# Kernel optimization log

Hardware: AMD Instinct MI355X
Metric: run time of the kernel (lower is better)

Reference implementation:

```python
import jax, jax.numpy as jnp
import numpy as np

WS = 11          # window_size
SIGMA = 1.5
PAD = (WS - 1) // 2
C1 = (0.01 * 1.0) ** 2
C2 = (0.03 * 1.0) ** 2


def _gaussian_kernel2d():
    # kornia-style: 1D gaussian over window, normalized, outer product
    x = jnp.arange(WS, dtype=jnp.float32) - WS // 2
    g = jnp.exp(-(x ** 2) / (2.0 * SIGMA ** 2))
    g = g / jnp.sum(g)
    return jnp.outer(g, g)  # [WS, WS]


def _filter2d(x, k2d):
    # depthwise 2D filter with reflect ('same') padding, as kornia.filter2D
    b, c, h, w = x.shape
    xp = jnp.pad(x, ((0, 0), (0, 0), (PAD, PAD), (PAD, PAD)), mode='reflect')
    kern = jnp.broadcast_to(k2d.astype(x.dtype), (c, 1, WS, WS))
    return jax.lax.conv_general_dilated(
        xp, kern, window_strides=(1, 1), padding='VALID',
        feature_group_count=c,
        dimension_numbers=('NCHW', 'OIHW', 'NCHW'))


def setup_inputs() -> dict:
    key = jax.random.key(0)
    k1, k2 = jax.random.split(key)
    inp = jax.random.normal(k1, (16, 1, 1024, 1024), dtype=jnp.float32)
    tgt = jax.random.uniform(k2, (16, 1, 1024, 1024), dtype=jnp.float32)
    return {"input": inp, "target": tgt}


def reference(input, target):
    k2d = _gaussian_kernel2d()
    img1 = jax.nn.sigmoid(input)  # logsigmoid(x).exp() == sigmoid(x)
    img2 = target

    mu1 = _filter2d(img1, k2d)
    mu2 = _filter2d(img2, k2d)
    mu1_sq = mu1 * mu1
    mu2_sq = mu2 * mu2
    mu1_mu2 = mu1 * mu2

    sigma1_sq = _filter2d(img1 * img1, k2d) - mu1_sq
    sigma2_sq = _filter2d(img2 * img2, k2d) - mu2_sq
    sigma12 = _filter2d(img1 * img2, k2d) - mu1_mu2

    ssim_map = ((2.0 * mu1_mu2 + C1) * (2.0 * sigma12 + C2)) / (
        (mu1_sq + mu2_sq + C1) * (sigma1_sq + sigma2_sq + C2))
    loss = jnp.clip(1.0 - ssim_map, 0.0, 1.0) / 2.0
    return jnp.mean(loss)  # reduction='mean'
```

## Files before the change

### kernel.cpp

```cpp
#include <hip/hip_runtime.h>
#include <math.h>


typedef __attribute__((ext_vector_type(2))) float f2;

#define H_IMG 1024
#define W_IMG 1024
#define N_IMG 16
#define TILE_W 256
#define TILE_H 128
#define PADR 5
#define LDS_S2 268

constexpr float GW[11] = {
    0.00102838f, 0.00759877f, 0.03600077f, 0.10936069f, 0.21300553f,
    0.26601172f,
    0.21300553f, 0.10936069f, 0.03600077f, 0.00759877f, 0.00102838f};

__device__ __forceinline__ int reflect_i(int i, int n) {
    i = (i < 0) ? -i : i;
    i = (i >= n) ? (2 * n - 2 - i) : i;
    return i;
}

__device__ __forceinline__ float fast_sigmoid(float x) {
    return __builtin_amdgcn_rcpf(1.0f + __expf(-x));
}

__device__ __forceinline__ void ssim_emit(
    f2 mu, f2 sq, float e12, float& loss_sum)
{
    const float mu1 = mu.x, mu2 = mu.y;
    const float mu1s = mu1 * mu1;
    const float mu2s = mu2 * mu2;
    const float mu12 = mu1 * mu2;
    const float s1  = sq.x - mu1s;
    const float s2  = sq.y - mu2s;
    const float s12 = e12  - mu12;
    const float C1 = 1e-4f, C2 = 9e-4f;
    const float num = (2.0f * mu12 + C1) * (2.0f * s12 + C2);
    const float den = (mu1s + mu2s + C1) * (s1 + s2 + C2);
    float l = 1.0f - num * __builtin_amdgcn_rcpf(den);
    l = fminf(fmaxf(l, 0.0f), 1.0f) * 0.5f;
    loss_sum += l;
}

template<int NR>
__device__ __forceinline__ void load_group(
    const float* __restrict__ A, const float* __restrict__ B,
    int y_start, int gb, int c0, int c1, int tid,
    float (&pa)[11], float (&pb)[11], float (&pa2)[11], float (&pb2)[11])
{
#pragma unroll
    for (int r = 0; r < NR; ++r) {
        const int yy = reflect_i(y_start + gb + r, H_IMG);
        const size_t ro = (size_t)yy * W_IMG;
        pa[r] = A[ro + c0];
        pb[r] = B[ro + c0];
        if (tid < 2 * PADR) {
            pa2[r] = A[ro + c1];
            pb2[r] = B[ro + c1];
        }
    }
}

template<int NR>
__device__ __forceinline__ void write_group(
    f2 (*__restrict__ buf)[LDS_S2], int tid,
    const float (&pa)[11], const float (&pb)[11],
    const float (&pa2)[11], const float (&pb2)[11])
{
#pragma unroll
    for (int r = 0; r < NR; ++r) {
        buf[r][tid] = (f2){fast_sigmoid(pa[r]), pb[r]};
        if (tid < 2 * PADR)
            buf[r][TILE_W + tid] = (f2){fast_sigmoid(pa2[r]), pb2[r]};
    }
}

template<int NR, bool GUARD>
__device__ __forceinline__ void process_group(
    const f2 (*__restrict__ buf)[LDS_S2], int tid,
    f2 (&vAB)[11], f2 (&vSQ)[11], float (&vX)[11], float& loss_sum)
{
#pragma unroll
    for (int r = 0; r < NR; ++r) {
        f2 hAB = (f2)(0.0f), hSQ = (f2)(0.0f);
        float hab = 0.0f;
#pragma unroll
        for (int k = 0; k < 11; ++k) {
            const f2 v   = buf[r][tid + k];
            const f2 wa2 = ((f2)(GW[k])) * v;
            hAB += wa2;
            hSQ  = __builtin_elementwise_fma(wa2, v, hSQ);
            hab  = fmaf(wa2.x, v.y, hab);
        }
#pragma unroll
        for (int j = 0; j < 11; ++j) {
            if (!(GUARD && j > r)) {
                const int s = (r - j + 22) % 11;
                const f2 w2 = (f2)(GW[j]);
                vAB[s] = __builtin_elementwise_fma(w2, hAB, vAB[s]);
                vSQ[s] = __builtin_elementwise_fma(w2, hSQ, vSQ[s]);
                vX[s]  = fmaf(GW[j], hab, vX[s]);
            }
        }
        if (!GUARD || r == 10) {
            const int s = (r + 1) % 11;
            ssim_emit(vAB[s], vSQ[s], vX[s], loss_sum);
            vAB[s] = (f2)(0.0f); vSQ[s] = (f2)(0.0f); vX[s] = 0.0f;
        }
    }
}

__global__ __launch_bounds__(256, 2) void ssim_main(
    const float* __restrict__ inp, const float* __restrict__ tgt,
    float* __restrict__ out)
{
    __shared__ f2 bufs[2][11][LDS_S2];
    __shared__ float red[4];

    const int tid = threadIdx.x;
    const int blk = blockIdx.x;
    const int b   = blk >> 5;
    const int rem = blk & 31;
    const int cx  = rem & 3;
    const int ry  = rem >> 2;
    const int x0  = cx * TILE_W;
    const int y0  = ry * TILE_H;

    const float* __restrict__ A = inp + (size_t)b * (H_IMG * (size_t)W_IMG);
    const float* __restrict__ B = tgt + (size_t)b * (H_IMG * (size_t)W_IMG);

    const int c0 = reflect_i(x0 - PADR + tid, W_IMG);
    const int c1 = (tid < 2 * PADR) ? reflect_i(x0 + TILE_W - PADR + tid, W_IMG) : 0;

    f2 vAB[11], vSQ[11];
    float vX[11];
#pragma unroll
    for (int j = 0; j < 11; ++j) {
        vAB[j] = (f2)(0.0f); vSQ[j] = (f2)(0.0f); vX[j] = 0.0f;
    }
    float pa[11], pb[11], pa2[11], pb2[11];
    float loss_sum = 0.0f;

    const int y_start = y0 - PADR;

    load_group<11>(A, B, y_start, 0, c0, c1, tid, pa, pb, pa2, pb2);
    write_group<11>(bufs[0], tid, pa, pb, pa2, pb2);
    load_group<11>(A, B, y_start, 11, c0, c1, tid, pa, pb, pa2, pb2);
    __syncthreads();
    process_group<11, true>(bufs[0], tid, vAB, vSQ, vX, loss_sum);

#pragma unroll 1
    for (int g = 1; g <= 11; ++g) {
        f2 (*cur)[LDS_S2] = bufs[g & 1];
        write_group<11>(cur, tid, pa, pb, pa2, pb2);
        if (g <= 10)
            load_group<11>(A, B, y_start, (g + 1) * 11, c0, c1, tid, pa, pb, pa2, pb2);
        else
            load_group<6>(A, B, y_start, 132, c0, c1, tid, pa, pb, pa2, pb2);
        __syncthreads();
        process_group<11, false>(cur, tid, vAB, vSQ, vX, loss_sum);
    }

    write_group<6>(bufs[0], tid, pa, pb, pa2, pb2);
    __syncthreads();
    process_group<6, false>(bufs[0], tid, vAB, vSQ, vX, loss_sum);

#pragma unroll
    for (int off = 32; off > 0; off >>= 1)
        loss_sum += __shfl_down(loss_sum, off, 64);
    const int wave = tid >> 6;
    if ((tid & 63) == 0) red[wave] = loss_sum;
    __syncthreads();
    if (tid == 0) {
        const float s = red[0] + red[1] + red[2] + red[3];
        atomicAdd(out, s * (1.0f / ((float)N_IMG * H_IMG * W_IMG)));
    }
}

extern "C" void kernel_launch(void* const* d_in, const int* in_sizes, int n_in,
                              void* d_out, int out_size, void* d_ws, size_t ws_size,
                              hipStream_t stream) {
    const float* inp = (const float*)d_in[0];
    const float* tgt = (const float*)d_in[1];
    float* out = (float*)d_out;

    hipMemsetAsync(out, 0, sizeof(float), stream);

    const int grid = N_IMG * 4 * (H_IMG / TILE_H);
    ssim_main<<<grid, 256, 0, stream>>>(inp, tgt, out);
}
```

Before: 182.7 us.

## Stream rows via global_load_lds DMA into a 12-slot ring with smaller tiles

Replaces register-staged global loads with direct global-to-LDS DMA into double-buffered 6-row slabs. Each slab is then repacked, with the sigmoid applied, into a 12-slot ring buffer that feeds the separable Gaussian accumulation. Tile height drops from 128 to 32 rows, quadrupling the block count, and the occupancy hint rises to 3 blocks per CU. This is meant to free registers, overlap memory with compute and improve latency hiding. In exchange, each block recomputes a larger 10-row halo relative to its height, and the manual waitcnt/barrier sequencing adds correctness risk.

Result: slower. 258.7 us (+41.6%).

```diff
diff --git a/kernel.cpp b/kernel.cpp
--- a/kernel.cpp
+++ b/kernel.cpp
@@ -8,9 +8,11 @@
 #define W_IMG 1024
 #define N_IMG 16
 #define TILE_W 256
-#define TILE_H 128
+#define TILE_H 32
 #define PADR 5
-#define LDS_S2 268
+#define RING_S 268
+#define SLAB_S 268
+#define NSLOT 12
 
 constexpr float GW[11] = {
     0.00102838f, 0.00759877f, 0.03600077f, 0.10936069f, 0.21300553f,
@@ -45,134 +47,158 @@
     loss_sum += l;
 }
 
-template<int NR>
-__device__ __forceinline__ void load_group(
-    const float* __restrict__ A, const float* __restrict__ B,
-    int y_start, int gb, int c0, int c1, int tid,
-    float (&pa)[11], float (&pb)[11], float (&pa2)[11], float (&pb2)[11])
+__device__ __forceinline__ void dma_f32(const float* gsrc, float* ldst) {
+    __builtin_amdgcn_global_load_lds(
+        (const __attribute__((address_space(1))) void*)gsrc,
+        (__attribute__((address_space(3))) void*)ldst, 4, 0, 0);
+}
+
+#define BAR_VM()   asm volatile("s_waitcnt vmcnt(0)\n\ts_barrier" ::: "memory")
+#define BAR_LGKM() asm volatile("s_waitcnt lgkmcnt(0)\n\ts_barrier" ::: "memory")
+
+struct Ctx {
+    const float* A;
+    const float* B;
+    float (*slab)[6][2][SLAB_S];
+    f2 (*ring)[RING_S];
+    int tid, lane, wv, c0, c1, y_start;
+};
+
+__device__ __forceinline__ void issue_dma6(const Ctx& cx, int base_row, int buf) {
+#pragma unroll
+    for (int i = 0; i < 6; ++i) {
+        const int y = reflect_i(cx.y_start + base_row + i, H_IMG);
+        const float* rowA = cx.A + ((size_t)y << 10);
+        const float* rowB = cx.B + ((size_t)y << 10);
+        dma_f32(rowA + cx.c0, &cx.slab[buf][i][0][cx.wv * 64]);
+        dma_f32(rowB + cx.c0, &cx.slab[buf][i][1][cx.wv * 64]);
+        if (cx.lane < 2 * PADR) {
+            dma_f32(rowA + cx.c1, &cx.slab[buf][i][0][256]);
+            dma_f32(rowB + cx.c1, &cx.slab[buf][i][1][256]);
+        }
+    }
+}
+
+template<int B0>
+__device__ __forceinline__ void repack6(const Ctx& cx, int buf) {
+#pragma unroll
+    for (int i = 0; i < 6; ++i) {
+        const int slot = (B0 + i) % NSLOT;
+        const float a = cx.slab[buf][i][0][cx.tid];
+        const float b = cx.slab[buf][i][1][cx.tid];
+        cx.ring[slot][cx.tid] = (f2){fast_sigmoid(a), b};
+        if (cx.tid < 2 * PADR) {
+            const float a2 = cx.slab[buf][i][0][256 + cx.tid];
+            const float b2 = cx.slab[buf][i][1][256 + cx.tid];
+            cx.ring[slot][256 + cx.tid] = (f2){fast_sigmoid(a2), b2};
+        }
+    }
+}
+
+template<int B0, bool GUARD>
+__device__ __forceinline__ void process6(
+    const Ctx& cx, f2 (&vAB)[NSLOT], f2 (&vSQ)[NSLOT], float (&vX)[NSLOT],
+    float& loss_sum)
 {
 #pragma unroll
-    for (int r = 0; r < NR; ++r) {
-        const int yy = reflect_i(y_start + gb + r, H_IMG);
-        const size_t ro = (size_t)yy * W_IMG;
-        pa[r] = A[ro + c0];
-        pb[r] = B[ro + c0];
-        if (tid < 2 * PADR) {
-            pa2[r] = A[ro + c1];
-            pb2[r] = B[ro + c1];
-        }
-    }
-}
-
-template<int NR>
-__device__ __forceinline__ void write_group(
-    f2 (*__restrict__ buf)[LDS_S2], int tid,
-    const float (&pa)[11], const float (&pb)[11],
-    const float (&pa2)[11], const float (&pb2)[11])
-{
-#pragma unroll
-    for (int r = 0; r < NR; ++r) {
-        buf[r][tid] = (f2){fast_sigmoid(pa[r]), pb[r]};
-        if (tid < 2 * PADR)
-            buf[r][TILE_W + tid] = (f2){fast_sigmoid(pa2[r]), pb2[r]};
-    }
-}
-
-template<int NR, bool GUARD>
-__device__ __forceinline__ void process_group(
-    const f2 (*__restrict__ buf)[LDS_S2], int tid,
-    f2 (&vAB)[11], f2 (&vSQ)[11], float (&vX)[11], float& loss_sum)
-{
-#pragma unroll
-    for (int r = 0; r < NR; ++r) {
+    for (int i = 0; i < 6; ++i) {
+        const int RR = B0 + i;
         f2 hAB = (f2)(0.0f), hSQ = (f2)(0.0f);
         float hab = 0.0f;
 #pragma unroll
         for (int k = 0; k < 11; ++k) {
-            const f2 v   = buf[r][tid + k];
-            const f2 wa2 = ((f2)(GW[k])) * v;
-            hAB += wa2;
-            hSQ  = __builtin_elementwise_fma(wa2, v, hSQ);
-            hab  = fmaf(wa2.x, v.y, hab);
+            const f2 v  = cx.ring[RR][cx.tid + k];
+            const f2 w2 = ((f2)(GW[k])) * v;
+            hAB += w2;
+            hSQ  = __builtin_elementwise_fma(w2, v, hSQ);
+            hab  = fmaf(w2.x, v.y, hab);
         }
 #pragma unroll
         for (int j = 0; j < 11; ++j) {
-            if (!(GUARD && j > r)) {
-                const int s = (r - j + 22) % 11;
-                const f2 w2 = (f2)(GW[j]);
-                vAB[s] = __builtin_elementwise_fma(w2, hAB, vAB[s]);
-                vSQ[s] = __builtin_elementwise_fma(w2, hSQ, vSQ[s]);
+            if (!(GUARD && j > RR)) {
+                const int s = (RR - j + 24) % NSLOT;
+                const f2 w = (f2)(GW[j]);
+                vAB[s] = __builtin_elementwise_fma(w, hAB, vAB[s]);
+                vSQ[s] = __builtin_elementwise_fma(w, hSQ, vSQ[s]);
                 vX[s]  = fmaf(GW[j], hab, vX[s]);
             }
         }
-        if (!GUARD || r == 10) {
-            const int s = (r + 1) % 11;
+        if (!GUARD || RR >= 10) {
+            const int s = (RR + 2) % NSLOT;
             ssim_emit(vAB[s], vSQ[s], vX[s], loss_sum);
             vAB[s] = (f2)(0.0f); vSQ[s] = (f2)(0.0f); vX[s] = 0.0f;
         }
     }
 }
 
-__global__ __launch_bounds__(256, 2) void ssim_main(
+__global__ __launch_bounds__(256, 3) void ssim_main(
     const float* __restrict__ inp, const float* __restrict__ tgt,
     float* __restrict__ out)
 {
-    __shared__ f2 bufs[2][11][LDS_S2];
+    __shared__ float slab[2][6][2][SLAB_S];
+    __shared__ f2 ring[NSLOT][RING_S];
     __shared__ float red[4];
 
-    const int tid = threadIdx.x;
+    const int tid  = threadIdx.x;
+    const int lane = tid & 63;
+    const int wv   = tid >> 6;
+
     const int blk = blockIdx.x;
-    const int b   = blk >> 5;
-    const int rem = blk & 31;
-    const int cx  = rem & 3;
+    const int img = blk >> 7;
+    const int rem = blk & 127;
+    const int cxt = rem & 3;
     const int ry  = rem >> 2;
-    const int x0  = cx * TILE_W;
+    const int x0  = cxt * TILE_W;
     const int y0  = ry * TILE_H;
 
-    const float* __restrict__ A = inp + (size_t)b * (H_IMG * (size_t)W_IMG);
-    const float* __restrict__ B = tgt + (size_t)b * (H_IMG * (size_t)W_IMG);
-
-    const int c0 = reflect_i(x0 - PADR + tid, W_IMG);
-    const int c1 = (tid < 2 * PADR) ? reflect_i(x0 + TILE_W - PADR + tid, W_IMG) : 0;
-
-    f2 vAB[11], vSQ[11];
-    float vX[11];
-#pragma unroll
-    for (int j = 0; j < 11; ++j) {
+    const float* A = inp + (size_t)img * (H_IMG * (size_t)W_IMG);
+    const float* B = tgt + (size_t)img * (H_IMG * (size_t)W_IMG);
+
+    Ctx cx;
+    cx.A = A; cx.B = B;
+    cx.slab = slab; cx.ring = ring;
+    cx.tid = tid; cx.lane = lane; cx.wv = wv;
+    cx.c0 = reflect_i(x0 - PADR + tid, W_IMG);
+    cx.c1 = reflect_i(x0 + 251 + lane, W_IMG);
+    cx.y_start = y0 - PADR;
+
+    f2 vAB[NSLOT], vSQ[NSLOT];
+    float vX[NSLOT];
+#pragma unroll
+    for (int j = 0; j < NSLOT; ++j) {
         vAB[j] = (f2)(0.0f); vSQ[j] = (f2)(0.0f); vX[j] = 0.0f;
     }
-    float pa[11], pb[11], pa2[11], pb2[11];
     float loss_sum = 0.0f;
 
-    const int y_start = y0 - PADR;
-
-    load_group<11>(A, B, y_start, 0, c0, c1, tid, pa, pb, pa2, pb2);
-    write_group<11>(bufs[0], tid, pa, pb, pa2, pb2);
-    load_group<11>(A, B, y_start, 11, c0, c1, tid, pa, pb, pa2, pb2);
+    issue_dma6(cx, 0, 0);
+
+    BAR_VM();  repack6<0>(cx, 0);  BAR_LGKM();
+    issue_dma6(cx, 6, 1);
+    process6<0, true>(cx, vAB, vSQ, vX, loss_sum);
+
+    BAR_VM();  repack6<6>(cx, 1);  BAR_LGKM();
+    issue_dma6(cx, 12, 0);
+    process6<6, true>(cx, vAB, vSQ, vX, loss_sum);
+
+#pragma unroll 1
+    for (int cb = 12; cb <= 24; cb += 12) {
+        BAR_VM();  repack6<0>(cx, 0);  BAR_LGKM();
+        issue_dma6(cx, cb + 6, 1);
+        process6<0, false>(cx, vAB, vSQ, vX, loss_sum);
+
+        BAR_VM();  repack6<6>(cx, 1);  BAR_LGKM();
+        issue_dma6(cx, cb + 12, 0);
+        process6<6, false>(cx, vAB, vSQ, vX, loss_sum);
+    }
+
+    BAR_VM();  repack6<0>(cx, 0);  BAR_LGKM();
+    process6<0, false>(cx, vAB, vSQ, vX, loss_sum);
+
     __syncthreads();
-    process_group<11, true>(bufs[0], tid, vAB, vSQ, vX, loss_sum);
-
-#pragma unroll 1
-    for (int g = 1; g <= 11; ++g) {
-        f2 (*cur)[LDS_S2] = bufs[g & 1];
-        write_group<11>(cur, tid, pa, pb, pa2, pb2);
-        if (g <= 10)
-            load_group<11>(A, B, y_start, (g + 1) * 11, c0, c1, tid, pa, pb, pa2, pb2);
-        else
-            load_group<6>(A, B, y_start, 132, c0, c1, tid, pa, pb, pa2, pb2);
-        __syncthreads();
-        process_group<11, false>(cur, tid, vAB, vSQ, vX, loss_sum);
-    }
-
-    write_group<6>(bufs[0], tid, pa, pb, pa2, pb2);
-    __syncthreads();
-    process_group<6, false>(bufs[0], tid, vAB, vSQ, vX, loss_sum);
-
 #pragma unroll
     for (int off = 32; off > 0; off >>= 1)
         loss_sum += __shfl_down(loss_sum, off, 64);
-    const int wave = tid >> 6;
-    if ((tid & 63) == 0) red[wave] = loss_sum;
+    if (lane == 0) red[wv] = loss_sum;
     __syncthreads();
     if (tid == 0) {
         const float s = red[0] + red[1] + red[2] + red[3];
```
